# Optimization experiments

Measured on AMD Instinct MI355X. Metric: run time of the kernel, lower is better.

Reference implementation:

```python
import jax, jax.numpy as jnp
import numpy as np

VOCAB = 81616
EMB = 32
B = 16384
NNZ = 200


def setup_inputs() -> dict:
    key = jax.random.key(0)
    k1, k2 = jax.random.split(key)
    indices = jax.random.randint(k1, (B, NNZ), 0, VOCAB, dtype=jnp.int32)
    values = jnp.ones((B, NNZ), dtype=jnp.float32)  # multi-hot sparse values
    w = jax.random.normal(k2, (VOCAB, EMB), dtype=jnp.float32) * 0.05
    b = jnp.zeros((EMB,), dtype=jnp.float32)
    return {"indices": indices, "values": values, "w": w, "b": b}


def reference(indices, values, w, b):
    # Equivalent to tf.matmul(tf.sparse.to_dense(inputs), w) + b, but computed
    # by gathering only the nonzero rows of the score matrix.
    # w[indices]: [B, NNZ, EMB]; weighted sum over NNZ -> [B, EMB]
    gathered = w[indices]
    out = jnp.einsum('bn,bne->be', values, gathered) + b
    return out
```

## Files before the change

kernel.cpp:

```cpp
#include <hip/hip_runtime.h>


constexpr int NNZ = 200;
constexpr int THREADS = 256;

__global__ __launch_bounds__(THREADS, 6) void playlist_embedding_kernel(
    const int* __restrict__ indices,
    const float* __restrict__ values,
    const float* __restrict__ w,
    const float* __restrict__ bias,
    float* __restrict__ out)
{
    const int tid    = threadIdx.x;
    const int wave   = tid >> 6;
    const int lane   = tid & 63;
    const int n_slot = lane >> 3;
    const int c      = lane & 7;

    const int row = blockIdx.x * 4 + wave;

    const int*   __restrict__ ri = indices + (size_t)row * NNZ;
    const float* __restrict__ rv = values  + (size_t)row * NNZ;
    const float4* __restrict__ w4 = (const float4*)w;

    float ax = 0.f, ay = 0.f, az = 0.f, aw = 0.f;

    #pragma unroll 5
    for (int k = 0; k < NNZ / 8; ++k) {
        const int n = n_slot + (k << 3);
        const int   u = ri[n];
        const float v = rv[n];
        const float4 wv = w4[(size_t)u * 8 + c];
        ax += v * wv.x;
        ay += v * wv.y;
        az += v * wv.z;
        aw += v * wv.w;
    }

    #pragma unroll
    for (int mask = 8; mask <= 32; mask <<= 1) {
        ax += __shfl_xor(ax, mask);
        ay += __shfl_xor(ay, mask);
        az += __shfl_xor(az, mask);
        aw += __shfl_xor(aw, mask);
    }

    if (n_slot == 0) {
        const float4 bias4 = ((const float4*)bias)[c];
        float4 o;
        o.x = ax + bias4.x;
        o.y = ay + bias4.y;
        o.z = az + bias4.z;
        o.w = aw + bias4.w;
        ((float4*)out)[(size_t)row * 8 + c] = o;
    }
}

extern "C" void kernel_launch(void* const* d_in, const int* in_sizes, int n_in,
                              void* d_out, int out_size, void* d_ws, size_t ws_size,
                              hipStream_t stream) {
    const int*   indices = (const int*)d_in[0];
    const float* values  = (const float*)d_in[1];
    const float* w       = (const float*)d_in[2];
    const float* bias    = (const float*)d_in[3];
    float* out = (float*)d_out;

    const int B = in_sizes[0] / NNZ;
    const int grid = B / 4;

    playlist_embedding_kernel<<<grid, THREADS, 0, stream>>>(
        indices, values, w, bias, out);
}
```

Before: 46.85 us.

## Software-pipeline index loads and embedding gathers with vectorized int4 index reads

Each wave now reads indices and values as int4/float4 chunks of four consecutive entries per lane group, which cuts the number of index-load instructions. It also runs a 3-slot software pipeline: indices are loaded two stages ahead and embedding rows are gathered one stage ahead of the FMAs. The goal is to put more independent gathers in flight per wave and hide global-memory latency. In exchange, more registers are live, so the launch bounds drop from 6 to 4 blocks per SM-equivalent, and the last stage uses a masked partial chunk.

```diff
diff --git a/kernel.cpp b/kernel.cpp
--- a/kernel.cpp
+++ b/kernel.cpp
@@ -3,49 +3,80 @@
 
 constexpr int NNZ = 200;
 constexpr int THREADS = 256;
+constexpr int ROWS_PER_BLOCK = 4;
+constexpr int NSTAGE = 7;
 
-__global__ __launch_bounds__(THREADS, 6) void playlist_embedding_kernel(
+__global__ __launch_bounds__(THREADS, 4) void playlist_embedding_kernel(
     const int* __restrict__ indices,
     const float* __restrict__ values,
     const float* __restrict__ w,
     const float* __restrict__ bias,
     float* __restrict__ out)
 {
-    const int tid    = threadIdx.x;
-    const int wave   = tid >> 6;
-    const int lane   = tid & 63;
-    const int n_slot = lane >> 3;
-    const int c      = lane & 7;
+    const int tid  = threadIdx.x;
+    const int wave = tid >> 6;
+    const int lane = tid & 63;
+    const int s    = lane >> 3;
+    const int c    = lane & 7;
 
-    const int row = blockIdx.x * 4 + wave;
+    const int row = blockIdx.x * ROWS_PER_BLOCK + wave;
 
     const int*   __restrict__ ri = indices + (size_t)row * NNZ;
     const float* __restrict__ rv = values  + (size_t)row * NNZ;
     const float4* __restrict__ w4 = (const float4*)w;
 
+    int4   id[3];
+    float4 vl[3];
+    float4 gb[3][4];
     float ax = 0.f, ay = 0.f, az = 0.f, aw = 0.f;
 
-    #pragma unroll 5
-    for (int k = 0; k < NNZ / 8; ++k) {
-        const int n = n_slot + (k << 3);
-        const int   u = ri[n];
-        const float v = rv[n];
-        const float4 wv = w4[(size_t)u * 8 + c];
-        ax += v * wv.x;
-        ay += v * wv.y;
-        az += v * wv.z;
-        aw += v * wv.w;
+    auto loadiv = [&](int slot, int k) {
+        int off;
+        if (k < 6) off = 32 * k + 4 * s;
+        else       off = 192 + ((s < 2) ? 4 * s : 0);
+        id[slot] = *(const int4*)(ri + off);
+        float4 t = *(const float4*)(rv + off);
+        if (k == 6 && s >= 2) { t.x = 0.f; t.y = 0.f; t.z = 0.f; t.w = 0.f; }
+        vl[slot] = t;
+    };
+    auto gather = [&](int slot) {
+        gb[slot][0] = w4[id[slot].x * 8 + c];
+        gb[slot][1] = w4[id[slot].y * 8 + c];
+        gb[slot][2] = w4[id[slot].z * 8 + c];
+        gb[slot][3] = w4[id[slot].w * 8 + c];
+    };
+    auto fmas = [&](int slot) {
+        const float4 v = vl[slot];
+        ax += v.x * gb[slot][0].x; ay += v.x * gb[slot][0].y;
+        az += v.x * gb[slot][0].z; aw += v.x * gb[slot][0].w;
+        ax += v.y * gb[slot][1].x; ay += v.y * gb[slot][1].y;
+        az += v.y * gb[slot][1].z; aw += v.y * gb[slot][1].w;
+        ax += v.z * gb[slot][2].x; ay += v.z * gb[slot][2].y;
+        az += v.z * gb[slot][2].z; aw += v.z * gb[slot][2].w;
+        ax += v.w * gb[slot][3].x; ay += v.w * gb[slot][3].y;
+        az += v.w * gb[slot][3].z; aw += v.w * gb[slot][3].w;
+    };
+
+    loadiv(0, 0);
+    loadiv(1, 1);
+    gather(0);
+
+    #pragma unroll
+    for (int k = 0; k < NSTAGE; ++k) {
+        if (k + 2 < NSTAGE) loadiv((k + 2) % 3, k + 2);
+        if (k + 1 < NSTAGE) gather((k + 1) % 3);
+        fmas(k % 3);
     }
 
     #pragma unroll
-    for (int mask = 8; mask <= 32; mask <<= 1) {
-        ax += __shfl_xor(ax, mask);
-        ay += __shfl_xor(ay, mask);
-        az += __shfl_xor(az, mask);
-        aw += __shfl_xor(aw, mask);
+    for (int m = 8; m <= 32; m <<= 1) {
+        ax += __shfl_xor(ax, m);
+        ay += __shfl_xor(ay, m);
+        az += __shfl_xor(az, m);
+        aw += __shfl_xor(aw, m);
     }
 
-    if (n_slot == 0) {
+    if (s == 0) {
         const float4 bias4 = ((const float4*)bias)[c];
         float4 o;
         o.x = ax + bias4.x;
@@ -66,7 +97,7 @@
     float* out = (float*)d_out;
 
     const int B = in_sizes[0] / NNZ;
-    const int grid = B / 4;
+    const int grid = B / ROWS_PER_BLOCK;
 
     playlist_embedding_kernel<<<grid, THREADS, 0, stream>>>(
         indices, values, w, bias, out);
```

Result: faster. 45.64 us (-2.6%).

## Prefetch indices as int4 and double-buffer gathers with inline asm waits

Applied to the files above, without the earlier changes.

Each lane now loads its indices and values as int4/float4 vectors up front, with the 200-entry tail handled by zeroing the padded values. The embedding-row gathers are then issued through inline asm in two ping-ponged groups of four dwordx4 loads, using explicit vmcnt waits so FMAs on one group overlap the loads of the next. This aims to keep more gathers in flight per wave and cut the number of index and value load instructions. In exchange it lowers the launch-bounds occupancy hint and adds register pressure, and the hand-placed waits and scheduling barriers constrain the compiler.

```diff
diff --git a/kernel.cpp b/kernel.cpp
--- a/kernel.cpp
+++ b/kernel.cpp
@@ -4,48 +4,97 @@
 constexpr int NNZ = 200;
 constexpr int THREADS = 256;
 
-__global__ __launch_bounds__(THREADS, 6) void playlist_embedding_kernel(
+__global__ __launch_bounds__(THREADS, 4) void playlist_embedding_kernel(
     const int* __restrict__ indices,
     const float* __restrict__ values,
     const float* __restrict__ w,
     const float* __restrict__ bias,
     float* __restrict__ out)
 {
-    const int tid    = threadIdx.x;
-    const int wave   = tid >> 6;
-    const int lane   = tid & 63;
-    const int n_slot = lane >> 3;
-    const int c      = lane & 7;
-
-    const int row = blockIdx.x * 4 + wave;
+    const int tid  = threadIdx.x;
+    const int wave = tid >> 6;
+    const int lane = tid & 63;
+    const int s    = lane >> 3;
+    const int c    = lane & 7;
+    const int row  = blockIdx.x * 4 + wave;
 
     const int*   __restrict__ ri = indices + (size_t)row * NNZ;
     const float* __restrict__ rv = values  + (size_t)row * NNZ;
     const float4* __restrict__ w4 = (const float4*)w;
 
+    int4   id[7];
+    float4 vl[7];
+#pragma unroll
+    for (int k = 0; k < 7; ++k) {
+        const int off = (k < 6) ? (32 * k + 4 * s)
+                                : (192 + ((s < 2) ? 4 * s : 0));
+        id[k] = *(const int4*)(ri + off);
+        float4 t = *(const float4*)(rv + off);
+        if (k == 6 && s >= 2) { t.x = 0.f; t.y = 0.f; t.z = 0.f; t.w = 0.f; }
+        vl[k] = t;
+    }
+
+    asm volatile("s_waitcnt vmcnt(0)" ::: "memory");
+    __builtin_amdgcn_sched_barrier(0);
+
+    float4 A0, A1, A2, A3, B0, B1, B2, B3;
     float ax = 0.f, ay = 0.f, az = 0.f, aw = 0.f;
 
-    #pragma unroll 5
-    for (int k = 0; k < NNZ / 8; ++k) {
-        const int n = n_slot + (k << 3);
-        const int   u = ri[n];
-        const float v = rv[n];
-        const float4 wv = w4[(size_t)u * 8 + c];
-        ax += v * wv.x;
-        ay += v * wv.y;
-        az += v * wv.z;
-        aw += v * wv.w;
+#define GATHER(G0, G1, G2, G3, K) do {                                         \
+    const float4* a0_ = w4 + ((long)id[K].x * 8 + c);                          \
+    const float4* a1_ = w4 + ((long)id[K].y * 8 + c);                          \
+    const float4* a2_ = w4 + ((long)id[K].z * 8 + c);                          \
+    const float4* a3_ = w4 + ((long)id[K].w * 8 + c);                          \
+    asm volatile("global_load_dwordx4 %0, %1, off" : "=v"(G0) : "v"(a0_));     \
+    asm volatile("global_load_dwordx4 %0, %1, off" : "=v"(G1) : "v"(a1_));     \
+    asm volatile("global_load_dwordx4 %0, %1, off" : "=v"(G2) : "v"(a2_));     \
+    asm volatile("global_load_dwordx4 %0, %1, off" : "=v"(G3) : "v"(a3_));     \
+} while (0)
+
+#define FMAS(G0, G1, G2, G3, K) do {                                           \
+    const float4 v_ = vl[K];                                                   \
+    ax += v_.x * G0.x; ay += v_.x * G0.y; az += v_.x * G0.z; aw += v_.x * G0.w;\
+    ax += v_.y * G1.x; ay += v_.y * G1.y; az += v_.y * G1.z; aw += v_.y * G1.w;\
+    ax += v_.z * G2.x; ay += v_.z * G2.y; az += v_.z * G2.z; aw += v_.z * G2.w;\
+    ax += v_.w * G3.x; ay += v_.w * G3.y; az += v_.w * G3.z; aw += v_.w * G3.w;\
+} while (0)
+
+#define WAIT4() do {                                                           \
+    asm volatile("s_waitcnt vmcnt(4)" ::: "memory");                           \
+    __builtin_amdgcn_sched_barrier(0);                                         \
+} while (0)
+
+#define WAIT0() do {                                                           \
+    asm volatile("s_waitcnt vmcnt(0)" ::: "memory");                           \
+    __builtin_amdgcn_sched_barrier(0);                                         \
+} while (0)
+
+    GATHER(A0, A1, A2, A3, 0);
+
+    GATHER(B0, B1, B2, B3, 1); WAIT4(); FMAS(A0, A1, A2, A3, 0);
+    GATHER(A0, A1, A2, A3, 2); WAIT4(); FMAS(B0, B1, B2, B3, 1);
+    GATHER(B0, B1, B2, B3, 3); WAIT4(); FMAS(A0, A1, A2, A3, 2);
+    GATHER(A0, A1, A2, A3, 4); WAIT4(); FMAS(B0, B1, B2, B3, 3);
+    GATHER(B0, B1, B2, B3, 5); WAIT4(); FMAS(A0, A1, A2, A3, 4);
+    GATHER(A0, A1, A2, A3, 6); WAIT4(); FMAS(B0, B1, B2, B3, 5);
+                               WAIT0(); FMAS(A0, A1, A2, A3, 6);
+
+#undef GATHER
+#undef FMAS
+#undef WAIT4
+#undef WAIT0
+
+    asm volatile("" ::: "memory");
+
+#pragma unroll
+    for (int m = 8; m <= 32; m <<= 1) {
+        ax += __shfl_xor(ax, m);
+        ay += __shfl_xor(ay, m);
+        az += __shfl_xor(az, m);
+        aw += __shfl_xor(aw, m);
     }
 
-    #pragma unroll
-    for (int mask = 8; mask <= 32; mask <<= 1) {
-        ax += __shfl_xor(ax, mask);
-        ay += __shfl_xor(ay, mask);
-        az += __shfl_xor(az, mask);
-        aw += __shfl_xor(aw, mask);
-    }
-
-    if (n_slot == 0) {
+    if (s == 0) {
         const float4 bias4 = ((const float4*)bias)[c];
         float4 o;
         o.x = ax + bias4.x;
```

Result: faster. 45.49 us (-2.9%).

## Gather bf16-converted weights with vocab-split bucketing and software-pipelined loads

Applied to the files above, without the earlier changes.

Each call first converts the fp32 weight table to bf16 in the workspace, which halves the bytes fetched per gathered row. The main kernel sorts each row's indices into two vocab halves through LDS using ballot and mbcnt, so that gathers touch a narrower address range at a time. It then issues the dwordx2 gathers in double-buffered batches with explicit vmcnt waits, and each wave handles four rows. This adds a conversion pass over the whole table on every call and rounds the weights to bf16, which lowers accuracy.

```diff
diff --git a/kernel.cpp b/kernel.cpp
--- a/kernel.cpp
+++ b/kernel.cpp
@@ -3,55 +3,185 @@
 
 constexpr int NNZ = 200;
 constexpr int THREADS = 256;
-
-__global__ __launch_bounds__(THREADS, 6) void playlist_embedding_kernel(
+constexpr int VOCAB = 81616;
+constexpr int EMB = 32;
+constexpr int SPLIT = 40960;
+constexpr int ROWS_PER_WAVE = 4;
+constexpr size_t WBF_BYTES = (size_t)VOCAB * EMB * 2;
+
+__global__ __launch_bounds__(256) void convert_w_bf16(
+    const float* __restrict__ w, unsigned short* __restrict__ o, int n)
+{
+    int i = blockIdx.x * blockDim.x + threadIdx.x;
+    if (i * 8 >= n) return;
+    const uint4 a = ((const uint4*)w)[i * 2 + 0];
+    const uint4 b = ((const uint4*)w)[i * 2 + 1];
+    auto cv = [](unsigned u) -> unsigned {
+        return (u + 0x7FFFu + ((u >> 16) & 1u)) >> 16;
+    };
+    uint4 p;
+    p.x = cv(a.x) | (cv(a.y) << 16);
+    p.y = cv(a.z) | (cv(a.w) << 16);
+    p.z = cv(b.x) | (cv(b.y) << 16);
+    p.w = cv(b.z) | (cv(b.w) << 16);
+    ((uint4*)o)[i] = p;
+}
+
+__global__ __launch_bounds__(THREADS, 4) void pe_bf16_tiled(
     const int* __restrict__ indices,
     const float* __restrict__ values,
-    const float* __restrict__ w,
+    const unsigned short* __restrict__ wb,
     const float* __restrict__ bias,
     float* __restrict__ out)
 {
-    const int tid    = threadIdx.x;
-    const int wave   = tid >> 6;
-    const int lane   = tid & 63;
-    const int n_slot = lane >> 3;
-    const int c      = lane & 7;
-
-    const int row = blockIdx.x * 4 + wave;
+    __shared__ unsigned long long bkt[4][NNZ];
+
+    const int tid  = threadIdx.x;
+    const int wv   = tid >> 6;
+    const int lane = tid & 63;
+    const int s    = lane >> 3;
+    const int c    = lane & 7;
+    unsigned long long* __restrict__ B = bkt[wv];
+
+    for (int rr = 0; rr < ROWS_PER_WAVE; ++rr) {
+        const int row = blockIdx.x * (4 * ROWS_PER_WAVE) + wv * ROWS_PER_WAVE + rr;
+        const int*   __restrict__ ri = indices + (size_t)row * NNZ;
+        const float* __restrict__ rv = values  + (size_t)row * NNZ;
+
+        int left = 0, right = 0;
+#pragma unroll
+        for (int j = 0; j < 4; ++j) {
+            const int n = j * 64 + lane;
+            const bool valid = (n < NNZ);
+            int iv = 0; float vvf = 0.f;
+            if (valid) {
+                iv  = __builtin_nontemporal_load(ri + n);
+                vvf = __builtin_nontemporal_load(rv + n);
+            }
+            const bool b0 = valid && (iv <  SPLIT);
+            const bool b1 = valid && (iv >= SPLIT);
+            const unsigned long long m0 = __ballot(b0);
+            const unsigned long long m1 = __ballot(b1);
+            const int bel0 = __builtin_amdgcn_mbcnt_hi(
+                (unsigned)(m0 >> 32), __builtin_amdgcn_mbcnt_lo((unsigned)m0, 0));
+            const int bel1 = __builtin_amdgcn_mbcnt_hi(
+                (unsigned)(m1 >> 32), __builtin_amdgcn_mbcnt_lo((unsigned)m1, 0));
+            if (valid) {
+                const int slot = b0 ? (left + bel0) : (NNZ - 1 - (right + bel1));
+                B[slot] = ((unsigned long long)__float_as_uint(vvf) << 32) | (unsigned)iv;
+            }
+            left  += __popcll(m0);
+            right += __popcll(m1);
+        }
+        const int cnt0 = left;
+        const int gap  = NNZ - right - cnt0;
+
+        asm volatile("s_waitcnt vmcnt(0)" ::: "memory");
+        __builtin_amdgcn_sched_barrier(0);
+
+        float ax = 0.f, ay = 0.f, az = 0.f, aw = 0.f;
+        uint2 GA[8], GB[8];
+        float VA[8], VB[8];
+
+#define ISSUE(K, G, V) do {                                                    \
+    _Pragma("unroll")                                                          \
+    for (int e = 0; e < 8; ++e) {                                              \
+        const int q = (K) * 64 + s * 8 + e;                                    \
+        const bool tval = ((K) < 3) || (q < NNZ);                              \
+        int sl = (q < cnt0) ? q : q + gap;                                     \
+        if (!tval) sl = 0;                                                     \
+        const unsigned long long ent = B[sl];                                  \
+        const int iv = (int)(unsigned)ent;                                     \
+        V[e] = tval ? __uint_as_float((unsigned)(ent >> 32)) : 0.f;            \
+        const unsigned short* a_ = wb + ((size_t)iv * 32 + c * 4);             \
+        asm volatile("global_load_dwordx2 %0, %1, off"                         \
+                     : "=v"(G[e]) : "v"(a_));                                  \
+    }                                                                          \
+} while (0)
+
+#define FMA8(G, V) do {                                                        \
+    _Pragma("unroll")                                                          \
+    for (int e = 0; e < 8; ++e) {                                              \
+        const float f0 = __uint_as_float(G[e].x << 16);                        \
+        const float f1 = __uint_as_float(G[e].x & 0xFFFF0000u);                \
+        const float f2 = __uint_as_float(G[e].y << 16);                        \
+        const float f3 = __uint_as_float(G[e].y & 0xFFFF0000u);                \
+        ax += V[e] * f0; ay += V[e] * f1;                                      \
+        az += V[e] * f2; aw += V[e] * f3;                                      \
+    }                                                                          \
+} while (0)
+
+#define WAITV(N) do {                                                          \
+    asm volatile("s_waitcnt vmcnt(" #N ")" ::: "memory");                      \
+    __builtin_amdgcn_sched_barrier(0);                                         \
+} while (0)
+
+        ISSUE(0, GA, VA);
+        ISSUE(1, GB, VB);
+        WAITV(8);  FMA8(GA, VA);
+        ISSUE(2, GA, VA);
+        WAITV(8);  FMA8(GB, VB);
+        ISSUE(3, GB, VB);
+        WAITV(8);  FMA8(GA, VA);
+        WAITV(0);  FMA8(GB, VB);
+
+#undef ISSUE
+#undef FMA8
+#undef WAITV
+
+        asm volatile("" ::: "memory");
+
+#pragma unroll
+        for (int m = 8; m <= 32; m <<= 1) {
+            ax += __shfl_xor(ax, m);
+            ay += __shfl_xor(ay, m);
+            az += __shfl_xor(az, m);
+            aw += __shfl_xor(aw, m);
+        }
+        if (s == 0) {
+            const float4 b4 = ((const float4*)bias)[c];
+            float4 o;
+            o.x = ax + b4.x; o.y = ay + b4.y;
+            o.z = az + b4.z; o.w = aw + b4.w;
+            ((float4*)out)[(size_t)row * 8 + c] = o;
+        }
+    }
+}
+
+__global__ __launch_bounds__(THREADS, 4) void pe_fp32_direct(
+    const int* __restrict__ indices, const float* __restrict__ values,
+    const float* __restrict__ w, const float* __restrict__ bias,
+    float* __restrict__ out)
+{
+    const int tid  = threadIdx.x;
+    const int wave = tid >> 6;
+    const int lane = tid & 63;
+    const int s    = lane >> 3;
+    const int c    = lane & 7;
+    const int row  = blockIdx.x * 4 + wave;
 
     const int*   __restrict__ ri = indices + (size_t)row * NNZ;
     const float* __restrict__ rv = values  + (size_t)row * NNZ;
     const float4* __restrict__ w4 = (const float4*)w;
 
     float ax = 0.f, ay = 0.f, az = 0.f, aw = 0.f;
-
-    #pragma unroll 5
+#pragma unroll 5
     for (int k = 0; k < NNZ / 8; ++k) {
-        const int n = n_slot + (k << 3);
+        const int n = s + (k << 3);
         const int   u = ri[n];
         const float v = rv[n];
         const float4 wv = w4[(size_t)u * 8 + c];
-        ax += v * wv.x;
-        ay += v * wv.y;
-        az += v * wv.z;
-        aw += v * wv.w;
-    }
-
-    #pragma unroll
-    for (int mask = 8; mask <= 32; mask <<= 1) {
-        ax += __shfl_xor(ax, mask);
-        ay += __shfl_xor(ay, mask);
-        az += __shfl_xor(az, mask);
-        aw += __shfl_xor(aw, mask);
-    }
-
-    if (n_slot == 0) {
-        const float4 bias4 = ((const float4*)bias)[c];
+        ax += v * wv.x; ay += v * wv.y; az += v * wv.z; aw += v * wv.w;
+    }
+#pragma unroll
+    for (int m = 8; m <= 32; m <<= 1) {
+        ax += __shfl_xor(ax, m); ay += __shfl_xor(ay, m);
+        az += __shfl_xor(az, m); aw += __shfl_xor(aw, m);
+    }
+    if (s == 0) {
+        const float4 b4 = ((const float4*)bias)[c];
         float4 o;
-        o.x = ax + bias4.x;
-        o.y = ay + bias4.y;
-        o.z = az + bias4.z;
-        o.w = aw + bias4.w;
+        o.x = ax + b4.x; o.y = ay + b4.y; o.z = az + b4.z; o.w = aw + b4.w;
         ((float4*)out)[(size_t)row * 8 + c] = o;
     }
 }
@@ -66,8 +196,16 @@
     float* out = (float*)d_out;
 
     const int B = in_sizes[0] / NNZ;
-    const int grid = B / 4;
-
-    playlist_embedding_kernel<<<grid, THREADS, 0, stream>>>(
-        indices, values, w, bias, out);
-}
+
+    if (ws_size >= WBF_BYTES) {
+        unsigned short* wb = (unsigned short*)d_ws;
+        const int nelem = VOCAB * EMB;
+        const int cgrid = (nelem / 8 + 255) / 256;
+        convert_w_bf16<<<cgrid, 256, 0, stream>>>(w, wb, nelem);
+
+        const int grid = B / (4 * ROWS_PER_WAVE);
+        pe_bf16_tiled<<<grid, THREADS, 0, stream>>>(indices, values, wb, bias, out);
+    } else {
+        pe_fp32_direct<<<B / 4, THREADS, 0, stream>>>(indices, values, w, bias, out);
+    }
+}
```

New measurement: 91.68 us. +95.7%, slower.
